# Performance work log

Hardware: AMD Instinct MI355X
Metric: run time of the kernel (lower is better)

Reference implementation:

```python
import jax, jax.numpy as jnp
import numpy as np

N_TOKENS, MODEL_DIM, NUM_EXPERTS = 65536, 1024, 64
CAPACITY_FACTOR = 1.0


def setup_inputs() -> dict:
    key = jax.random.key(0)
    k1, k2 = jax.random.split(key)
    x = jax.random.normal(k1, (N_TOKENS, MODEL_DIM), dtype=jnp.float32)
    # gate projection weight, torch Linear stores [out_features, in_features]
    wg = jax.random.normal(k2, (NUM_EXPERTS, MODEL_DIM), dtype=jnp.float32) * (1.0 / np.sqrt(MODEL_DIM))
    return {"x": x, "wg": wg}


def reference(x, wg):
    N, E = x.shape[0], wg.shape[0]
    logits = x @ wg.T                              # [N, E]
    # training-branch capacity: capacity_factor * ceil(N / E)
    capacity = int(CAPACITY_FACTOR * ((N + E - 1) // E))
    indices1_s = jnp.argmax(logits, axis=1)        # [N] top-1 expert per token
    gates = jax.nn.softmax(logits, axis=1)         # [N, E]
    mask1 = jax.nn.one_hot(indices1_s, E, dtype=gates.dtype)  # [N, E]
    gates1_s = jnp.sum(gates * mask1, axis=1)      # [N] gate value of chosen expert
    # locations1_s[i] = number of earlier tokens routed to the same expert
    # (exclusive prefix count = inclusive cumsum - 1 at the selected column)
    locations1 = jnp.cumsum(mask1, axis=0) - 1.0   # [N, E]
    locations1_s = jnp.sum(locations1 * mask1, axis=1).astype(jnp.int32)
    # auxiliary load-balance loss (float32 branch of the original)
    me = jnp.sum(gates, axis=0)                    # [E]
    ce = jnp.sum(mask1, axis=0)                    # [E]
    l_aux = jnp.sum(me * ce) * (E / (N * N))
    return (l_aux, indices1_s.astype(jnp.int32), capacity, locations1_s, gates1_s, E)
```

## Files before the change

kernel.cpp:

```cpp
#include <hip/hip_runtime.h>

#define NT 65536
#define MD 1024
#define NE 64
#define BK 32
#define NBLK (NT / 64)

__global__ __launch_bounds__(256) void gate_kernel(
    const float* __restrict__ x, const float* __restrict__ wg,
    float* __restrict__ out, unsigned* __restrict__ packed_ws,
    int* __restrict__ hist_ws, float* __restrict__ me)
{
    __shared__ __align__(16) float smem[4 * BK * 68];
    float (*as)[BK][68] = (float (*)[BK][68])smem;
    float (*bs)[BK][68] = (float (*)[BK][68])(smem + 2 * BK * 68);

    const int tid = threadIdx.x;
    const int tx = tid & 15;
    const int ty = tid >> 4;
    const int t0 = blockIdx.x * 64;

    const int r0 = tid >> 3, q0 = tid & 7;
    const int r1 = r0 + 32,  q1 = q0;
    const float* xa0 = x  + (size_t)(t0 + r0) * MD + q0 * 4;
    const float* xa1 = x  + (size_t)(t0 + r1) * MD + q1 * 4;
    const float* wa0 = wg + (size_t)r0 * MD + q0 * 4;
    const float* wa1 = wg + (size_t)r1 * MD + q1 * 4;

    float4 va0 = *(const float4*)(xa0);
    float4 va1 = *(const float4*)(xa1);
    float4 vw0 = *(const float4*)(wa0);
    float4 vw1 = *(const float4*)(wa1);

#define STAGE(buf)                                                      \
    do {                                                                \
        as[buf][q0 * 4 + 0][r0] = va0.x; as[buf][q0 * 4 + 1][r0] = va0.y; \
        as[buf][q0 * 4 + 2][r0] = va0.z; as[buf][q0 * 4 + 3][r0] = va0.w; \
        as[buf][q1 * 4 + 0][r1] = va1.x; as[buf][q1 * 4 + 1][r1] = va1.y; \
        as[buf][q1 * 4 + 2][r1] = va1.z; as[buf][q1 * 4 + 3][r1] = va1.w; \
        bs[buf][q0 * 4 + 0][r0] = vw0.x; bs[buf][q0 * 4 + 1][r0] = vw0.y; \
        bs[buf][q0 * 4 + 2][r0] = vw0.z; bs[buf][q0 * 4 + 3][r0] = vw0.w; \
        bs[buf][q1 * 4 + 0][r1] = vw1.x; bs[buf][q1 * 4 + 1][r1] = vw1.y; \
        bs[buf][q1 * 4 + 2][r1] = vw1.z; bs[buf][q1 * 4 + 3][r1] = vw1.w; \
    } while (0)

    STAGE(0);
    __syncthreads();

    float acc[4][4];
#pragma unroll
    for (int i = 0; i < 4; ++i)
#pragma unroll
        for (int j = 0; j < 4; ++j) acc[i][j] = 0.f;

    for (int it = 0; it < MD / BK; ++it) {
        const int cur = it & 1;
        if (it < MD / BK - 1) {
            const int kn = (it + 1) * BK;
            va0 = *(const float4*)(xa0 + kn);
            va1 = *(const float4*)(xa1 + kn);
            vw0 = *(const float4*)(wa0 + kn);
            vw1 = *(const float4*)(wa1 + kn);
        }
#pragma unroll
        for (int k = 0; k < BK; ++k) {
            float4 a = *(const float4*)&as[cur][k][ty * 4];
            float4 b = *(const float4*)&bs[cur][k][tx * 4];
            float av[4] = {a.x, a.y, a.z, a.w};
            float bv[4] = {b.x, b.y, b.z, b.w};
#pragma unroll
            for (int i = 0; i < 4; ++i)
#pragma unroll
                for (int j = 0; j < 4; ++j) acc[i][j] += av[i] * bv[j];
        }
        if (it < MD / BK - 1) {
            const int nb = cur ^ 1;
            STAGE(nb);
        }
        __syncthreads();
    }

    float* lt  = smem;
    float* inv = smem + 4160;

#pragma unroll
    for (int i = 0; i < 4; ++i)
#pragma unroll
        for (int j = 0; j < 4; ++j)
            lt[(ty * 4 + i) * 65 + tx * 4 + j] = acc[i][j];
    __syncthreads();

    if (tid < 64) {
        const int t = tid;
        float m = -1e30f; int am = 0;
        for (int e = 0; e < NE; ++e) {
            float v = lt[t * 65 + e];
            if (v > m) { m = v; am = e; }
        }
        float s = 0.f;
        for (int e = 0; e < NE; ++e) {
            float ev = __expf(lt[t * 65 + e] - m);
            lt[t * 65 + e] = ev;
            s += ev;
        }
        float g = 1.0f / s;
        const int gt = t0 + t;
        out[1 + gt] = (float)am;
        out[2 + 2 * NT + gt] = g;
        inv[t] = g;

        const unsigned long long below = (1ull << t) - 1ull;
        int rank = 0, mycnt = 0;
        for (int e = 0; e < NE; ++e) {
            unsigned long long msk = __ballot(am == e);
            if (t == e)  mycnt = (int)__popcll(msk);
            if (am == e) rank  = (int)__popcll(msk & below);
        }
        packed_ws[gt] = (unsigned)am | ((unsigned)rank << 8);
        hist_ws[blockIdx.x * NE + t] = mycnt;
    }
    __syncthreads();

    if (tid < NE) {
        const int e = tid;
        float s = 0.f;
        for (int t = 0; t < 64; ++t) s += lt[t * 65 + e] * inv[t];
        atomicAdd(&me[e], s);
    }
}

__global__ __launch_bounds__(256) void scan_kernel(
    int* __restrict__ hist_ws, float* __restrict__ ce)
{
    const int e = blockIdx.x;
    const int tid = threadIdx.x;
    const int lane = tid & 63, wave = tid >> 6;
    __shared__ int wtot[4];

    int h[4];
#pragma unroll
    for (int j = 0; j < 4; ++j) h[j] = hist_ws[(tid * 4 + j) * NE + e];
    int s = h[0] + h[1] + h[2] + h[3];

    int scan = s;
#pragma unroll
    for (int d = 1; d < 64; d <<= 1) {
        int o = __shfl_up(scan, d, 64);
        if (lane >= d) scan += o;
    }
    if (lane == 63) wtot[wave] = scan;
    __syncthreads();
    int wpre = 0;
#pragma unroll
    for (int w = 0; w < 4; ++w)
        if (w < wave) wpre += wtot[w];

    int run = wpre + scan - s;
#pragma unroll
    for (int j = 0; j < 4; ++j) {
        hist_ws[(tid * 4 + j) * NE + e] = run;
        run += h[j];
    }
    if (tid == 255) ce[e] = (float)run;
}

__global__ __launch_bounds__(256) void emit_kernel(
    const unsigned* __restrict__ packed_ws, const int* __restrict__ offs_ws,
    float* __restrict__ out)
{
    const int i = blockIdx.x * 256 + threadIdx.x;
    const unsigned p = packed_ws[i];
    const int am = (int)(p & 63u);
    const int rank = (int)(p >> 8);
    const int b = i >> 6;
    out[2 + NT + i] = (float)(offs_ws[b * NE + am] + rank);
}

__global__ void finalize_kernel(const float* __restrict__ me,
                                const float* __restrict__ ce,
                                float* __restrict__ out)
{
    int tid = threadIdx.x;
    float v = me[tid] * ce[tid];
#pragma unroll
    for (int d = 32; d > 0; d >>= 1) v += __shfl_down(v, d, 64);
    if (tid == 0) {
        out[0] = v * (float)((double)NE / ((double)NT * (double)NT));
        out[1 + NT] = 1024.0f;
        out[2 + 3 * NT] = 64.0f;
    }
}

extern "C" void kernel_launch(void* const* d_in, const int* in_sizes, int n_in,
                              void* d_out, int out_size, void* d_ws, size_t ws_size,
                              hipStream_t stream)
{
    const float* x  = (const float*)d_in[0];
    const float* wg = (const float*)d_in[1];
    float* out = (float*)d_out;

    unsigned* packed_ws = (unsigned*)d_ws;
    int* hist_ws = (int*)((char*)d_ws + (size_t)NT * 4);
    float* me = (float*)((char*)d_ws + (size_t)NT * 4 + (size_t)NBLK * NE * 4);
    float* ce = me + NE;

    hipMemsetAsync(me, 0, NE * sizeof(float), stream);
    gate_kernel<<<NBLK, 256, 0, stream>>>(x, wg, out, packed_ws, hist_ws, me);
    scan_kernel<<<NE, 256, 0, stream>>>(hist_ws, ce);
    emit_kernel<<<NT / 256, 256, 0, stream>>>(packed_ws, hist_ws, out);
    finalize_kernel<<<1, 64, 0, stream>>>(me, ce, out);
}
```

Baseline: 408.3 us.

## Compute gate logits with split-bf16 MFMA emulating fp32 precision

Replaces the scalar fp32 SIMT GEMM with bf16 MFMA instructions, splitting each fp32 operand into three bf16 parts and summing six cross-products to keep near-fp32 accuracy. A prep kernel pre-splits and re-lays out the gate weights into MFMA fragment order in workspace. Each block now handles 128 tokens, with x read straight from global memory and no LDS staging. The finalize kernel is folded into the emit kernel to drop one launch. Argmax ties could flip if the emulated precision differs slightly from the fp32 reference.

```diff
diff --git a/kernel.cpp b/kernel.cpp
--- a/kernel.cpp
+++ b/kernel.cpp
@@ -3,111 +3,155 @@
 #define NT 65536
 #define MD 1024
 #define NE 64
-#define BK 32
-#define NBLK (NT / 64)
-
-__global__ __launch_bounds__(256) void gate_kernel(
-    const float* __restrict__ x, const float* __restrict__ wg,
+#define TB 128
+#define NGATE (NT / TB)
+#define NGRP (NT / 64)
+
+typedef short bf16x8 __attribute__((ext_vector_type(8)));
+typedef float f32x4  __attribute__((ext_vector_type(4)));
+
+__device__ __forceinline__ void split1(float f, ushort& h, ushort& m, ushort& lo) {
+    unsigned u  = __float_as_uint(f);
+    unsigned hb = u & 0xFFFF0000u;
+    float    r1 = f - __uint_as_float(hb);
+    unsigned mb = __float_as_uint(r1) & 0xFFFF0000u;
+    float    r2 = r1 - __uint_as_float(mb);
+    h  = (ushort)(hb >> 16);
+    m  = (ushort)(mb >> 16);
+    lo = (ushort)(__float_as_uint(r2) >> 16);
+}
+
+__device__ __forceinline__ void split8(const float4 a, const float4 b,
+                                       bf16x8& h, bf16x8& m, bf16x8& lo) {
+    float f[8] = {a.x, a.y, a.z, a.w, b.x, b.y, b.z, b.w};
+#pragma unroll
+    for (int j = 0; j < 8; ++j) {
+        ushort hh, mm, ll;
+        split1(f[j], hh, mm, ll);
+        h[j] = (short)hh; m[j] = (short)mm; lo[j] = (short)ll;
+    }
+}
+
+__global__ __launch_bounds__(256) void prep_kernel(
+    const float* __restrict__ wg, ushort* __restrict__ wgp)
+{
+    const int idx = blockIdx.x * 256 + threadIdx.x;
+    const int l  = idx & 63;
+    const int nt = (idx >> 6) & 3;
+    const int c  = idx >> 8;
+    const int e  = nt * 16 + (l & 15);
+    const int k0 = c * 32 + (l >> 4) * 8;
+    const float* src = wg + (size_t)e * MD + k0;
+    float4 a = *(const float4*)(src);
+    float4 b = *(const float4*)(src + 4);
+    bf16x8 h, m, lo;
+    split8(a, b, h, m, lo);
+    *(bf16x8*)(wgp + (size_t)idx * 8)          = h;
+    *(bf16x8*)(wgp + 65536 + (size_t)idx * 8)  = m;
+    *(bf16x8*)(wgp + 131072 + (size_t)idx * 8) = lo;
+}
+
+#define MFMA6(accv, xh, xm, xl, wh, wm, wl)                                        \
+    accv = __builtin_amdgcn_mfma_f32_16x16x32_bf16(xh, wh, accv, 0, 0, 0);         \
+    accv = __builtin_amdgcn_mfma_f32_16x16x32_bf16(xh, wm, accv, 0, 0, 0);         \
+    accv = __builtin_amdgcn_mfma_f32_16x16x32_bf16(xm, wh, accv, 0, 0, 0);         \
+    accv = __builtin_amdgcn_mfma_f32_16x16x32_bf16(xm, wm, accv, 0, 0, 0);         \
+    accv = __builtin_amdgcn_mfma_f32_16x16x32_bf16(xh, wl, accv, 0, 0, 0);         \
+    accv = __builtin_amdgcn_mfma_f32_16x16x32_bf16(xl, wh, accv, 0, 0, 0);
+
+__global__ __launch_bounds__(256, 2) void gate_kernel(
+    const float* __restrict__ x, const ushort* __restrict__ wgp,
     float* __restrict__ out, unsigned* __restrict__ packed_ws,
     int* __restrict__ hist_ws, float* __restrict__ me)
 {
-    __shared__ __align__(16) float smem[4 * BK * 68];
-    float (*as)[BK][68] = (float (*)[BK][68])smem;
-    float (*bs)[BK][68] = (float (*)[BK][68])(smem + 2 * BK * 68);
+    __shared__ float lt[TB * 65];
+    __shared__ float inv[TB];
 
     const int tid = threadIdx.x;
-    const int tx = tid & 15;
-    const int ty = tid >> 4;
-    const int t0 = blockIdx.x * 64;
-
-    const int r0 = tid >> 3, q0 = tid & 7;
-    const int r1 = r0 + 32,  q1 = q0;
-    const float* xa0 = x  + (size_t)(t0 + r0) * MD + q0 * 4;
-    const float* xa1 = x  + (size_t)(t0 + r1) * MD + q1 * 4;
-    const float* wa0 = wg + (size_t)r0 * MD + q0 * 4;
-    const float* wa1 = wg + (size_t)r1 * MD + q1 * 4;
-
-    float4 va0 = *(const float4*)(xa0);
-    float4 va1 = *(const float4*)(xa1);
-    float4 vw0 = *(const float4*)(wa0);
-    float4 vw1 = *(const float4*)(wa1);
-
-#define STAGE(buf)                                                      \
-    do {                                                                \
-        as[buf][q0 * 4 + 0][r0] = va0.x; as[buf][q0 * 4 + 1][r0] = va0.y; \
-        as[buf][q0 * 4 + 2][r0] = va0.z; as[buf][q0 * 4 + 3][r0] = va0.w; \
-        as[buf][q1 * 4 + 0][r1] = va1.x; as[buf][q1 * 4 + 1][r1] = va1.y; \
-        as[buf][q1 * 4 + 2][r1] = va1.z; as[buf][q1 * 4 + 3][r1] = va1.w; \
-        bs[buf][q0 * 4 + 0][r0] = vw0.x; bs[buf][q0 * 4 + 1][r0] = vw0.y; \
-        bs[buf][q0 * 4 + 2][r0] = vw0.z; bs[buf][q0 * 4 + 3][r0] = vw0.w; \
-        bs[buf][q1 * 4 + 0][r1] = vw1.x; bs[buf][q1 * 4 + 1][r1] = vw1.y; \
-        bs[buf][q1 * 4 + 2][r1] = vw1.z; bs[buf][q1 * 4 + 3][r1] = vw1.w; \
-    } while (0)
-
-    STAGE(0);
+    const int wv  = tid >> 6;
+    const int l   = tid & 63;
+    const int lr  = l & 15;
+    const int lg  = l >> 4;
+    const int t0  = blockIdx.x * TB + wv * 32;
+
+    const float*  xa0 = x + (size_t)(t0 + lr) * MD + lg * 8;
+    const float*  xa1 = xa0 + 16 * MD;
+    const ushort* wbh = wgp + (size_t)l * 8;
+    const ushort* wbm = wbh + 65536;
+    const ushort* wbl = wbh + 131072;
+
+    f32x4 acc[2][4];
+#pragma unroll
+    for (int mt = 0; mt < 2; ++mt)
+#pragma unroll
+        for (int nt = 0; nt < 4; ++nt) acc[mt][nt] = f32x4{0.f, 0.f, 0.f, 0.f};
+
+    float4 a00 = *(const float4*)(xa0);
+    float4 a01 = *(const float4*)(xa0 + 4);
+    float4 a10 = *(const float4*)(xa1);
+    float4 a11 = *(const float4*)(xa1 + 4);
+
+#pragma unroll 2
+    for (int c = 0; c < 32; ++c) {
+        const ushort* ph = wbh + c * 2048;
+        const ushort* pm = wbm + c * 2048;
+        const ushort* pl = wbl + c * 2048;
+        bf16x8 bh[4], bm_[4], bl[4];
+#pragma unroll
+        for (int nt = 0; nt < 4; ++nt) {
+            bh[nt]  = *(const bf16x8*)(ph + nt * 512);
+            bm_[nt] = *(const bf16x8*)(pm + nt * 512);
+            bl[nt]  = *(const bf16x8*)(pl + nt * 512);
+        }
+        float4 c00 = a00, c01 = a01, c10 = a10, c11 = a11;
+        if (c < 31) {
+            const float* xn0 = xa0 + (c + 1) * 32;
+            const float* xn1 = xa1 + (c + 1) * 32;
+            a00 = *(const float4*)(xn0);
+            a01 = *(const float4*)(xn0 + 4);
+            a10 = *(const float4*)(xn1);
+            a11 = *(const float4*)(xn1 + 4);
+        }
+        bf16x8 ah0, am0, al0, ah1, am1, al1;
+        split8(c00, c01, ah0, am0, al0);
+        split8(c10, c11, ah1, am1, al1);
+#pragma unroll
+        for (int nt = 0; nt < 4; ++nt) {
+            MFMA6(acc[0][nt], ah0, am0, al0, bh[nt], bm_[nt], bl[nt]);
+            MFMA6(acc[1][nt], ah1, am1, al1, bh[nt], bm_[nt], bl[nt]);
+        }
+    }
+
+#pragma unroll
+    for (int mt = 0; mt < 2; ++mt)
+#pragma unroll
+        for (int nt = 0; nt < 4; ++nt)
+#pragma unroll
+            for (int r = 0; r < 4; ++r)
+                lt[(wv * 32 + mt * 16 + lg * 4 + r) * 65 + nt * 16 + lr] =
+                    acc[mt][nt][r];
     __syncthreads();
 
-    float acc[4][4];
-#pragma unroll
-    for (int i = 0; i < 4; ++i)
-#pragma unroll
-        for (int j = 0; j < 4; ++j) acc[i][j] = 0.f;
-
-    for (int it = 0; it < MD / BK; ++it) {
-        const int cur = it & 1;
-        if (it < MD / BK - 1) {
-            const int kn = (it + 1) * BK;
-            va0 = *(const float4*)(xa0 + kn);
-            va1 = *(const float4*)(xa1 + kn);
-            vw0 = *(const float4*)(wa0 + kn);
-            vw1 = *(const float4*)(wa1 + kn);
-        }
-#pragma unroll
-        for (int k = 0; k < BK; ++k) {
-            float4 a = *(const float4*)&as[cur][k][ty * 4];
-            float4 b = *(const float4*)&bs[cur][k][tx * 4];
-            float av[4] = {a.x, a.y, a.z, a.w};
-            float bv[4] = {b.x, b.y, b.z, b.w};
-#pragma unroll
-            for (int i = 0; i < 4; ++i)
-#pragma unroll
-                for (int j = 0; j < 4; ++j) acc[i][j] += av[i] * bv[j];
-        }
-        if (it < MD / BK - 1) {
-            const int nb = cur ^ 1;
-            STAGE(nb);
-        }
-        __syncthreads();
-    }
-
-    float* lt  = smem;
-    float* inv = smem + 4160;
-
-#pragma unroll
-    for (int i = 0; i < 4; ++i)
-#pragma unroll
-        for (int j = 0; j < 4; ++j)
-            lt[(ty * 4 + i) * 65 + tx * 4 + j] = acc[i][j];
-    __syncthreads();
-
-    if (tid < 64) {
-        const int t = tid;
-        float m = -1e30f; int am = 0;
+    if (tid < 128) {
+        const int grp = tid >> 6;
+        const int t   = tid & 63;
+        float* row = &lt[(grp * 64 + t) * 65];
+        float mx = -1e30f; int am = 0;
         for (int e = 0; e < NE; ++e) {
-            float v = lt[t * 65 + e];
-            if (v > m) { m = v; am = e; }
+            float v = row[e];
+            if (v > mx) { mx = v; am = e; }
         }
         float s = 0.f;
         for (int e = 0; e < NE; ++e) {
-            float ev = __expf(lt[t * 65 + e] - m);
-            lt[t * 65 + e] = ev;
+            float ev = __expf(row[e] - mx);
+            row[e] = ev;
             s += ev;
         }
         float g = 1.0f / s;
-        const int gt = t0 + t;
+        const int gt = blockIdx.x * TB + grp * 64 + t;
         out[1 + gt] = (float)am;
         out[2 + 2 * NT + gt] = g;
-        inv[t] = g;
+        inv[grp * 64 + t] = g;
 
         const unsigned long long below = (1ull << t) - 1ull;
         int rank = 0, mycnt = 0;
@@ -117,14 +161,17 @@
             if (am == e) rank  = (int)__popcll(msk & below);
         }
         packed_ws[gt] = (unsigned)am | ((unsigned)rank << 8);
-        hist_ws[blockIdx.x * NE + t] = mycnt;
+        hist_ws[(blockIdx.x * 2 + grp) * NE + t] = mycnt;
     }
     __syncthreads();
 
-    if (tid < NE) {
-        const int e = tid;
+    if (tid < 128) {
+        const int grp = tid >> 6;
+        const int e   = tid & 63;
+        const float* base = &lt[grp * 64 * 65];
+        const float* iv   = &inv[grp * 64];
         float s = 0.f;
-        for (int t = 0; t < 64; ++t) s += lt[t * 65 + e] * inv[t];
+        for (int t = 0; t < 64; ++t) s += base[t * 65 + e] * iv[t];
         atomicAdd(&me[e], s);
     }
 }
@@ -166,6 +213,7 @@
 
 __global__ __launch_bounds__(256) void emit_kernel(
     const unsigned* __restrict__ packed_ws, const int* __restrict__ offs_ws,
+    const float* __restrict__ me, const float* __restrict__ ce,
     float* __restrict__ out)
 {
     const int i = blockIdx.x * 256 + threadIdx.x;
@@ -174,20 +222,16 @@
     const int rank = (int)(p >> 8);
     const int b = i >> 6;
     out[2 + NT + i] = (float)(offs_ws[b * NE + am] + rank);
-}
-
-__global__ void finalize_kernel(const float* __restrict__ me,
-                                const float* __restrict__ ce,
-                                float* __restrict__ out)
-{
-    int tid = threadIdx.x;
-    float v = me[tid] * ce[tid];
-#pragma unroll
-    for (int d = 32; d > 0; d >>= 1) v += __shfl_down(v, d, 64);
-    if (tid == 0) {
-        out[0] = v * (float)((double)NE / ((double)NT * (double)NT));
-        out[1 + NT] = 1024.0f;
-        out[2 + 3 * NT] = 64.0f;
+
+    if (blockIdx.x == 0 && threadIdx.x < 64) {
+        float v = me[threadIdx.x] * ce[threadIdx.x];
+#pragma unroll
+        for (int d = 32; d > 0; d >>= 1) v += __shfl_down(v, d, 64);
+        if (threadIdx.x == 0) {
+            out[0] = v * (float)((double)NE / ((double)NT * (double)NT));
+            out[1 + NT] = 1024.0f;
+            out[2 + 3 * NT] = 64.0f;
+        }
     }
 }
 
@@ -200,13 +244,14 @@
     float* out = (float*)d_out;
 
     unsigned* packed_ws = (unsigned*)d_ws;
-    int* hist_ws = (int*)((char*)d_ws + (size_t)NT * 4);
-    float* me = (float*)((char*)d_ws + (size_t)NT * 4 + (size_t)NBLK * NE * 4);
-    float* ce = me + NE;
+    int*      hist_ws   = (int*)((char*)d_ws + 262144);
+    float*    me        = (float*)((char*)d_ws + 524288);
+    float*    ce        = (float*)((char*)d_ws + 524544);
+    ushort*   wgp       = (ushort*)((char*)d_ws + 524800);
 
     hipMemsetAsync(me, 0, NE * sizeof(float), stream);
-    gate_kernel<<<NBLK, 256, 0, stream>>>(x, wg, out, packed_ws, hist_ws, me);
+    prep_kernel<<<32, 256, 0, stream>>>(wg, wgp);
+    gate_kernel<<<NGATE, 256, 0, stream>>>(x, wgp, out, packed_ws, hist_ws, me);
     scan_kernel<<<NE, 256, 0, stream>>>(hist_ws, ce);
-    emit_kernel<<<NT / 256, 256, 0, stream>>>(packed_ws, hist_ws, out);
-    finalize_kernel<<<1, 64, 0, stream>>>(me, ce, out);
-}
+    emit_kernel<<<NT / 256, 256, 0, stream>>>(packed_ws, hist_ws, me, ce, out);
+}
```

Measured after the change: 422.9 us. 1.04x slower.
